# Kernel optimization log

Measured on AMD Instinct MI355X. Metric: run time of the kernel, lower is better.

Reference implementation:

```python
import jax, jax.numpy as jnp
import numpy as np

B, CDD, HIS, S, E = 16, 5, 100, 30, 256
H, V, Qd, K = 16, 16, 200, 3
R = H * V            # repr_dim = 256
T = 2 * S + 1        # transformer_length = 61
VOCAB = 50000
TAU = 0.1


def setup_inputs() -> dict:
    key = jax.random.key(0)
    ks = jax.random.split(key, 14)
    s = lambda d: float(d) ** -0.5
    return {
        "candidate_title": jax.random.randint(ks[0], (B, CDD, S), 0, VOCAB, dtype=jnp.int32),
        "clicked_title": jax.random.randint(ks[1], (B, HIS, S), 0, VOCAB, dtype=jnp.int32),
        "his_mask": jnp.zeros((B, HIS, 1), dtype=bool),
        "candidate_title_pad": jnp.ones((B, CDD, S), jnp.float32),
        "clicked_title_pad": jnp.ones((B, HIS, S), jnp.float32),
        "embedding": jax.random.normal(ks[2], (VOCAB, E), jnp.float32) * 0.1,
        "Wq_words": jax.random.normal(ks[3], (H, E, E), jnp.float32) * s(E),
        "Wv_words": jax.random.normal(ks[4], (H, E, V), jnp.float32) * s(E),
        "Wk_words": jax.random.normal(ks[5], (R, Qd), jnp.float32) * s(R),
        "bk_words": jnp.zeros((Qd,), jnp.float32),
        "query_words": jax.random.normal(ks[6], (1, Qd), jnp.float32),
        "Wq_itrs": jax.random.normal(ks[7], (H, R, R), jnp.float32) * s(R),
        "Wv_itrs": jax.random.normal(ks[8], (H, R, V), jnp.float32) * s(R),
        "Wk_itrs": jax.random.normal(ks[9], (R, Qd), jnp.float32) * s(R),
        "bk_itrs": jnp.zeros((Qd,), jnp.float32),
        "query_itrs": jax.random.normal(ks[10], (1, Qd), jnp.float32),
        "W_ltr": jax.random.normal(ks[11], (R, 1), jnp.float32) * s(R),
        "b_ltr": jnp.zeros((1,), jnp.float32),
    }


def _mhsa(x, Wq, Wv, Wk, bk, qvec):
    """Batched multi-head self-attention + additive pooling.
    x: [..., L, D]; Wq: [H, D, D]; Wv: [H, D, V]; Wk: [H*V, Qd]; qvec: [1, Qd].
    NOTE: original always scales by 1/sqrt(embedding_dim), even in mode 2.
    """
    scale = 1.0 / jnp.sqrt(jnp.asarray(E, x.dtype))
    q = jnp.einsum('...ld,hde->h...le', x, Wq)                     # per-head query
    attn = jax.nn.softmax(jnp.einsum('h...le,...me->h...lm', q, x) * scale, axis=-1)
    ctx = jnp.einsum('h...lm,...md->h...ld', attn, x)
    val = jnp.einsum('h...ld,hdv->...lhv', ctx, Wv)                # head-major concat
    mv = val.reshape(val.shape[:-2] + (H * V,))                    # [..., L, R]
    keyp = jnp.tanh(mv @ Wk + bk)                                  # [..., L, Qd]
    w = jax.nn.softmax((keyp @ qvec[0]) * scale, axis=-1)          # additive attn [..., L]
    return jnp.einsum('...l,...lr->...r', w, mv), mv


def reference(candidate_title, clicked_title, his_mask, candidate_title_pad,
              clicked_title_pad, embedding, Wq_words, Wv_words, Wk_words,
              bk_words, query_words, Wq_itrs, Wv_itrs, Wk_itrs, bk_itrs,
              query_itrs, W_ltr, b_ltr):
    # news encoding (dropout_p = 0 -> identity)
    cdd_repr, cdd_emb = _mhsa(embedding[candidate_title], Wq_words, Wv_words,
                              Wk_words, bk_words, query_words)     # [B,CDD,R], [B,CDD,S,R]
    his_repr, his_emb = _mhsa(embedding[clicked_title], Wq_words, Wv_words,
                              Wk_words, bk_words, query_words)     # [B,HIS,R], [B,HIS,S,R]

    # news-level attention with greedy gumbel top-k selection
    logits = jnp.einsum('bcr,bhr->bch', cdd_repr, his_repr)        # [B,CDD,HIS]
    logits = jnp.where(jnp.swapaxes(his_mask, -1, -2), -jnp.inf, logits)
    gkey = jax.random.key(42)
    his_flat = his_emb.reshape(B, HIS, S * R)
    acts = []
    for i in range(K):
        g = jax.random.gumbel(jax.random.fold_in(gkey, i), logits.shape, logits.dtype)
        y = jax.nn.softmax((logits + g) / TAU, axis=-1)
        hard = jax.nn.one_hot(jnp.argmax(y, -1), HIS, dtype=y.dtype)
        focus = hard - jax.lax.stop_gradient(y) + y                # straight-through
        acts.append(jnp.einsum('bch,bhx->bcx', focus, his_flat).reshape(B, CDD, S, R))
        logits = jnp.where(hard > 0, -jnp.inf, logits)
    his_act = jnp.stack(acts, axis=2)                              # [B,CDD,K,S,R]

    # fusion: candidate words | zero separator | activated history words
    fusion = jnp.zeros((B, CDD, K, T, R), his_act.dtype)
    fusion = fusion.at[..., :S, :].set(jnp.broadcast_to(cdd_emb[:, :, None], (B, CDD, K, S, R)))
    fusion = fusion.at[..., S + 1:, :].set(his_act)
    fvec, _ = _mhsa(fusion, Wq_itrs, Wv_itrs, Wk_itrs, bk_itrs, query_itrs)  # [B,CDD,K,R]
    fvec = fvec.mean(axis=2)                                       # [B,CDD,R]

    score = (fvec @ W_ltr + b_ltr)[..., 0]                         # [B,CDD]
    return jax.nn.log_softmax(score, axis=1)
```

## Files before the change

### kernel.cpp

```cpp
#include <hip/hip_runtime.h>
#include <hip/hip_bf16.h>
#include <stdint.h>

#define BB    16
#define CDD   5
#define HIS   100
#define SS    30
#define EE    256
#define HH    16
#define VV    16
#define QD    200
#define KK    3
#define TT    61
#define NCAND 80
#define NITEM 1680
#define NFUS  240

typedef __attribute__((ext_vector_type(8))) short bf16x8;
typedef __attribute__((ext_vector_type(4))) float f32x4;
#define MFMA16(a, b, c) __builtin_amdgcn_mfma_f32_16x16x32_bf16(a, b, c, 0, 0, 0)

__device__ __forceinline__ int SWZ(int l, int c) { return l * 256 + (((c) ^ (l & 7)) << 2); }
__device__ __forceinline__ int SWZW(int l, int c) {
    return l * 256 + (((c ^ (l & 7) ^ ((l & 24) >> 1))) << 2);
}

__device__ __forceinline__ float dot4(float4 a, float4 b) {
    return a.x * b.x + a.y * b.y + a.z * b.z + a.w * b.w;
}
__device__ __forceinline__ uint32_t f2bf(float x) {
    uint32_t u = __float_as_uint(x);
    return (u + 0x7fffu + ((u >> 16) & 1u)) >> 16;
}
__device__ __forceinline__ uint32_t splitpack(float x) {
    uint32_t hb = f2bf(x);
    float hf = __uint_as_float(hb << 16);
    uint32_t lb = f2bf(x - hf);
    return (hb << 16) | lb;
}
union b8u4 { uint4 u; bf16x8 b; };
__device__ __forceinline__ bf16x8 hi8(uint4 a, uint4 b) {
    b8u4 cv;
    cv.u.x = (a.x >> 16) | (a.y & 0xffff0000u);
    cv.u.y = (a.z >> 16) | (a.w & 0xffff0000u);
    cv.u.z = (b.x >> 16) | (b.y & 0xffff0000u);
    cv.u.w = (b.z >> 16) | (b.w & 0xffff0000u);
    return cv.b;
}
__device__ __forceinline__ bf16x8 lo8(uint4 a, uint4 b) {
    b8u4 cv;
    cv.u.x = (a.x & 0xffffu) | (a.y << 16);
    cv.u.y = (a.z & 0xffffu) | (a.w << 16);
    cv.u.z = (b.x & 0xffffu) | (b.y << 16);
    cv.u.w = (b.z & 0xffffu) | (b.w << 16);
    return cv.b;
}

__device__ __forceinline__ uint32_t rotl32(uint32_t v, int r) {
    return (v << r) | (v >> (32 - r));
}
__device__ __forceinline__ void tf2x32(uint32_t k0, uint32_t k1, uint32_t& x0, uint32_t& x1) {
    uint32_t k2 = k0 ^ k1 ^ 0x1BD11BDAu;
    x0 += k0; x1 += k1;
    const int r0[4] = {13, 15, 26, 6}, r1[4] = {17, 29, 16, 24};
    #pragma unroll
    for (int i = 0; i < 4; ++i) { x0 += x1; x1 = rotl32(x1, r0[i]); x1 ^= x0; }
    x0 += k1; x1 += k2 + 1u;
    #pragma unroll
    for (int i = 0; i < 4; ++i) { x0 += x1; x1 = rotl32(x1, r1[i]); x1 ^= x0; }
    x0 += k2; x1 += k0 + 2u;
    #pragma unroll
    for (int i = 0; i < 4; ++i) { x0 += x1; x1 = rotl32(x1, r0[i]); x1 ^= x0; }
    x0 += k0; x1 += k1 + 3u;
    #pragma unroll
    for (int i = 0; i < 4; ++i) { x0 += x1; x1 = rotl32(x1, r1[i]); x1 ^= x0; }
    x0 += k1; x1 += k2 + 4u;
    #pragma unroll
    for (int i = 0; i < 4; ++i) { x0 += x1; x1 = rotl32(x1, r0[i]); x1 ^= x0; }
    x0 += k2; x1 += k0 + 5u;
}

__global__ __launch_bounds__(256) void ktrans(const float* __restrict__ Wk,
                                              float* __restrict__ WkT) {
    int j = blockIdx.x;
    int r = threadIdx.x;
    WkT[j * 256 + r] = Wk[r * QD + j];
}

__global__ __launch_bounds__(256) void kprep(const float* __restrict__ W,
                                             uint16_t* __restrict__ WF) {
    const int hkt = blockIdx.x;
    const int h = hkt >> 3, kt = hkt & 7;
    const int tid = threadIdx.x;
    const int l = tid & 63, nq = tid >> 6;
    const int g = l >> 4, ml = l & 15;
    for (int t = 0; t < 4; ++t) {
        int nt = nq * 4 + t;
        uint16_t* dst = WF + (((size_t)(h * 8 + kt) * 16 + nt) * 64 + l) * 16;
        #pragma unroll
        for (int i = 0; i < 8; ++i) {
            float x = W[(size_t)h * 65536 + (size_t)(kt * 32 + g * 8 + i) * 256 + nt * 16 + ml];
            uint32_t hb = f2bf(x);
            float hf = __uint_as_float(hb << 16);
            uint32_t lb = f2bf(x - hf);
            dst[i] = (uint16_t)hb;
            dst[8 + i] = (uint16_t)lb;
        }
    }
}

__global__ __launch_bounds__(64) void kprepv(const float* __restrict__ Wv,
                                             uint16_t* __restrict__ WF) {
    const int hkt = blockIdx.x;
    const int h = hkt >> 3, kt = hkt & 7;
    const int l = threadIdx.x;
    const int g = l >> 4, ml = l & 15;
    uint16_t* dst = WF + ((size_t)hkt * 64 + l) * 16;
    #pragma unroll
    for (int i = 0; i < 8; ++i) {
        float x = Wv[((size_t)h * 256 + kt * 32 + g * 8 + i) * 16 + ml];
        uint32_t hb = f2bf(x);
        float hf = __uint_as_float(hb << 16);
        uint32_t lb = f2bf(x - hf);
        dst[i] = (uint16_t)hb;
        dst[8 + i] = (uint16_t)lb;
    }
}

__global__ __launch_bounds__(256) void kword(
    const int* __restrict__ cand, const int* __restrict__ clk,
    const float* __restrict__ emb, const uint16_t* __restrict__ Wfrag,
    const uint16_t* __restrict__ WvF, const float* __restrict__ WkT,
    const float* __restrict__ bk, const float* __restrict__ qv,
    float* __restrict__ mv_out, float* __restrict__ repr_out)
{
    __shared__ __align__(16) uint32_t xsb[32 * 256];
    __shared__ __align__(16) uint32_t qs[32 * 256];
    __shared__ __align__(16) float ps[SS * 33];
    __shared__ __align__(16) float xv[32 * VV];
    __shared__ float scr[32];
    __shared__ float wts[32];

    const int item = blockIdx.x;
    const int tid  = threadIdx.x;
    const int w    = tid >> 6, lane = tid & 63;
    const int g    = lane >> 4, ml = lane & 15;
    const int* tok = (item < NCAND) ? cand + item * SS : clk + (item - NCAND) * SS;

    for (int p = tid; p < 32 * 64; p += 256) {
        int l = p >> 6, c = p & 63;
        float4 v = make_float4(0.f, 0.f, 0.f, 0.f);
        if (l < SS) v = *(const float4*)&emb[(size_t)tok[l] * EE + 4 * c];
        uint4 s;
        s.x = splitpack(v.x); s.y = splitpack(v.y);
        s.z = splitpack(v.z); s.w = splitpack(v.w);
        *(uint4*)&xsb[SWZW(l, c)] = s;
    }
    __syncthreads();

    float* mvg = mv_out + (size_t)item * SS * EE;

    for (int h = 0; h < HH; ++h) {
        {
            f32x4 acc[2][4];
            #pragma unroll
            for (int a = 0; a < 2; ++a)
                #pragma unroll
                for (int b = 0; b < 4; ++b) acc[a][b] = (f32x4){0.f, 0.f, 0.f, 0.f};
            const uint16_t* WH = Wfrag + (size_t)h * (8 * 16 * 64 * 16);
            for (int kt = 0; kt < 8; ++kt) {
                bf16x8 ah[2], al[2];
                #pragma unroll
                for (int mt = 0; mt < 2; ++mt) {
                    int row = mt * 16 + ml;
                    int c0 = kt * 8 + 2 * g;
                    uint4 A0 = *(const uint4*)&xsb[SWZW(row, c0)];
                    uint4 A1 = *(const uint4*)&xsb[SWZW(row, c0 + 1)];
                    ah[mt] = hi8(A0, A1);
                    al[mt] = lo8(A0, A1);
                }
                #pragma unroll
                for (int n2 = 0; n2 < 4; ++n2) {
                    const uint16_t* bp = WH + (((size_t)kt * 16 + (w * 4 + n2)) * 64 + lane) * 16;
                    bf16x8 bh = *(const bf16x8*)bp;
                    bf16x8 bl = *(const bf16x8*)(bp + 8);
                    #pragma unroll
                    for (int mt = 0; mt < 2; ++mt) {
                        acc[mt][n2] = MFMA16(ah[mt], bh, acc[mt][n2]);
                        acc[mt][n2] = MFMA16(al[mt], bh, acc[mt][n2]);
                        acc[mt][n2] = MFMA16(ah[mt], bl, acc[mt][n2]);
                        acc[mt][n2] = MFMA16(al[mt], bl, acc[mt][n2]);
                    }
                }
            }
            #pragma unroll
            for (int mt = 0; mt < 2; ++mt)
                #pragma unroll
                for (int n2 = 0; n2 < 4; ++n2) {
                    int col = (w * 4 + n2) * 16 + ml;
                    int chunk = col >> 2, sub = col & 3;
                    #pragma unroll
                    for (int r = 0; r < 4; ++r) {
                        int row = mt * 16 + g * 4 + r;
                        qs[row * 256 + (((chunk ^ (row & 7) ^ ((row & 24) >> 1)) << 2) | sub)] =
                            splitpack(acc[mt][n2][r]);
                    }
                }
        }
        __syncthreads();

        if (w < 2) {
            f32x4 accs[2];
            accs[0] = (f32x4){0.f, 0.f, 0.f, 0.f};
            accs[1] = (f32x4){0.f, 0.f, 0.f, 0.f};
            const int arow = 16 * w + ml;
            for (int kt = 0; kt < 8; ++kt) {
                int c0 = kt * 8 + 2 * g;
                uint4 Q0 = *(const uint4*)&qs[SWZW(arow, c0)];
                uint4 Q1 = *(const uint4*)&qs[SWZW(arow, c0 + 1)];
                bf16x8 qh = hi8(Q0, Q1), ql = lo8(Q0, Q1);
                #pragma unroll
                for (int nt = 0; nt < 2; ++nt) {
                    int brow = nt * 16 + ml;
                    uint4 X0 = *(const uint4*)&xsb[SWZW(brow, c0)];
                    uint4 X1 = *(const uint4*)&xsb[SWZW(brow, c0 + 1)];
                    bf16x8 xh = hi8(X0, X1), xl = lo8(X0, X1);
                    accs[nt] = MFMA16(qh, xh, accs[nt]);
                    accs[nt] = MFMA16(ql, xh, accs[nt]);
                    accs[nt] = MFMA16(qh, xl, accs[nt]);
                }
            }
            #pragma unroll
            for (int r = 0; r < 4; ++r) {
                float v0 = accs[0][r] * 0.0625f;
                float v1 = (ml < 14) ? accs[1][r] * 0.0625f : -INFINITY;
                float mx = fmaxf(v0, v1);
                mx = fmaxf(mx, __shfl_xor(mx, 1));
                mx = fmaxf(mx, __shfl_xor(mx, 2));
                mx = fmaxf(mx, __shfl_xor(mx, 4));
                mx = fmaxf(mx, __shfl_xor(mx, 8));
                float e0 = expf(v0 - mx);
                float e1 = (ml < 14) ? expf(v1 - mx) : 0.f;
                float s = e0 + e1;
                s += __shfl_xor(s, 1); s += __shfl_xor(s, 2);
                s += __shfl_xor(s, 4); s += __shfl_xor(s, 8);
                float inv = 1.f / s;
                int lrow = 16 * w + 4 * g + r;
                if (lrow < SS) {
                    ps[lrow * 33 + ml] = e0 * inv;
                    if (ml < 14) ps[lrow * 33 + 16 + ml] = e1 * inv;
                }
            }
        } else {
            f32x4 accv = (f32x4){0.f, 0.f, 0.f, 0.f};
            const int mt = w - 2;
            const int arow = 16 * mt + ml;
            for (int kt = 0; kt < 8; ++kt) {
                int c0 = kt * 8 + 2 * g;
                uint4 A0 = *(const uint4*)&xsb[SWZW(arow, c0)];
                uint4 A1 = *(const uint4*)&xsb[SWZW(arow, c0 + 1)];
                bf16x8 ah = hi8(A0, A1), al = lo8(A0, A1);
                const uint16_t* bp = WvF + (((size_t)h * 8 + kt) * 64 + lane) * 16;
                bf16x8 bh = *(const bf16x8*)bp;
                bf16x8 bl = *(const bf16x8*)(bp + 8);
                accv = MFMA16(ah, bh, accv);
                accv = MFMA16(al, bh, accv);
                accv = MFMA16(ah, bl, accv);
            }
            #pragma unroll
            for (int r = 0; r < 4; ++r) {
                int m = 16 * mt + 4 * g + r;
                if (m < SS) xv[m * 16 + ml] = accv[r];
            }
        }
        __syncthreads();

        if (tid < SS * 4) {
            const int l = tid >> 2, vq = tid & 3;
            float4 a = make_float4(0.f, 0.f, 0.f, 0.f);
            for (int m = 0; m < SS; ++m) {
                float pw = ps[l * 33 + m];
                float4 v4 = *(const float4*)&xv[m * 16 + vq * 4];
                a.x += pw * v4.x; a.y += pw * v4.y; a.z += pw * v4.z; a.w += pw * v4.w;
            }
            *(float4*)&mvg[l * 256 + h * 16 + vq * 4] = a;
        }
    }

    __threadfence();
    __syncthreads();
    float* kq = (float*)qs;
    if (tid < 200) {
        const int jq = tid % 50, lg = tid / 50;
        const int j0 = jq * 4;
        const int r0 = lg * 8;
        const int nr = (lg == 3) ? 6 : 8;
        float4 a[8];
        #pragma unroll
        for (int r = 0; r < 8; ++r) a[r] = make_float4(bk[j0], bk[j0+1], bk[j0+2], bk[j0+3]);
        for (int c = 0; c < 64; ++c) {
            float4 w0 = *(const float4*)&WkT[(j0 + 0) * 256 + 4 * c];
            float4 w1 = *(const float4*)&WkT[(j0 + 1) * 256 + 4 * c];
            float4 w2 = *(const float4*)&WkT[(j0 + 2) * 256 + 4 * c];
            float4 w3 = *(const float4*)&WkT[(j0 + 3) * 256 + 4 * c];
            #pragma unroll
            for (int r = 0; r < 8; ++r) {
                if (r < nr) {
                    float4 m4 = *(const float4*)&mvg[(r0 + r) * 256 + 4 * c];
                    a[r].x += dot4(m4, w0);
                    a[r].y += dot4(m4, w1);
                    a[r].z += dot4(m4, w2);
                    a[r].w += dot4(m4, w3);
                }
            }
        }
        #pragma unroll
        for (int r = 0; r < 8; ++r) {
            if (r < nr) {
                int row = r0 + r;
                kq[row * 204 + j0 + 0] = tanhf(a[r].x) * qv[j0 + 0];
                kq[row * 204 + j0 + 1] = tanhf(a[r].y) * qv[j0 + 1];
                kq[row * 204 + j0 + 2] = tanhf(a[r].z) * qv[j0 + 2];
                kq[row * 204 + j0 + 3] = tanhf(a[r].w) * qv[j0 + 3];
            }
        }
    }
    __syncthreads();
    if (tid < SS) {
        float a = 0.f;
        for (int j = 0; j < QD; ++j) a += kq[tid * 204 + j];
        scr[tid] = a * 0.0625f;
    }
    __syncthreads();
    if (tid == 0) {
        float mx = -INFINITY;
        for (int l = 0; l < SS; ++l) mx = fmaxf(mx, scr[l]);
        float sum = 0.f;
        for (int l = 0; l < SS; ++l) { float ev = expf(scr[l] - mx); wts[l] = ev; sum += ev; }
        float inv = 1.f / sum;
        for (int l = 0; l < SS; ++l) wts[l] *= inv;
    }
    __syncthreads();
    {
        float a = 0.f;
        for (int l = 0; l < SS; ++l) a += wts[l] * mvg[l * 256 + tid];
        repr_out[(size_t)item * EE + tid] = a;
    }
}

__global__ __launch_bounds__(128) void klogit(
    const float* __restrict__ repr, float* __restrict__ logits)
{
    const int bc = blockIdx.x;
    const int b  = bc / CDD;
    const int tid = threadIdx.x;
    __shared__ float cr[EE];
    for (int e = tid; e < EE; e += 128) cr[e] = repr[(size_t)bc * EE + e];
    __syncthreads();
    for (int h = tid; h < HIS; h += 128) {
        const float* hr = repr + (size_t)(NCAND + b * HIS + h) * EE;
        float a = 0.f;
        for (int e = 0; e < EE; ++e) a += cr[e] * hr[e];
        logits[bc * HIS + h] = a;
    }
}

__global__ __launch_bounds__(128) void ksel(
    const float* __restrict__ logits, int* __restrict__ sel)
{
    const int bc = blockIdx.x, tid = threadIdx.x;
    __shared__ float lg[HIS];
    __shared__ float pert[HIS];
    for (int h = tid; h < HIS; h += 128) lg[h] = logits[bc * HIS + h];
    __syncthreads();
    for (int i = 0; i < KK; ++i) {
        uint32_t c0 = 0u, c1 = (uint32_t)i;
        tf2x32(0u, 42u, c0, c1);
        for (int h = tid; h < HIS; h += 128) {
            int n = bc * HIS + h;
            uint32_t x0, x1; int lane;
            if (n < 4000) { x0 = (uint32_t)n;          x1 = (uint32_t)(n + 4000); lane = 0; }
            else          { x0 = (uint32_t)(n - 4000); x1 = (uint32_t)n;          lane = 1; }
            tf2x32(c0, c1, x0, x1);
            uint32_t bits = lane ? x1 : x0;
            float f = __uint_as_float((bits >> 9) | 0x3F800000u) - 1.0f;
            const float TINY = 1.17549435e-38f;
            float u = fmaxf(f + TINY, TINY);
            float g = -logf(-logf(u));
            pert[h] = lg[h] + g;
        }
        __syncthreads();
        if (tid == 0) {
            float best = -INFINITY; int bi = 0;
            for (int h = 0; h < HIS; ++h)
                if (pert[h] > best) { best = pert[h]; bi = h; }
            sel[bc * KK + i] = bi;
            lg[bi] = -INFINITY;
        }
        __syncthreads();
    }
}

__global__ __launch_bounds__(256) void kfus(
    const float* __restrict__ mv, const int* __restrict__ sel,
    const uint16_t* __restrict__ Wfrag, const uint16_t* __restrict__ WvF,
    float* __restrict__ mvf)
{
    __shared__ __align__(16) uint32_t xsb[64 * 256];
    __shared__ __align__(16) uint16_t qsb[64 * 256];
    __shared__ __align__(16) float ps[64 * 65];
    __shared__ __align__(16) float xv[64 * 16];

    const int item = blockIdx.x;
    const int tid  = threadIdx.x;
    const int w    = tid >> 6, lane = tid & 63;
    const int g    = lane >> 4, ml = lane & 15;
    const int bc = item / KK, k = item - bc * KK;
    const int b  = bc / CDD;
    const int sh = sel[bc * KK + k];
    const float* cmv = mv + (size_t)bc * SS * EE;
    const float* hmv = mv + (size_t)(NCAND + b * HIS + sh) * SS * EE;
    float* out = mvf + (size_t)item * TT * EE;

    for (int p = tid; p < 64 * 64; p += 256) {
        int l = p >> 6, c = p & 63;
        float4 v = make_float4(0.f, 0.f, 0.f, 0.f);
        if (l < SS)                v = *(const float4*)&cmv[l * 256 + 4 * c];
        else if (l > SS && l < TT) v = *(const float4*)&hmv[(l - SS - 1) * 256 + 4 * c];
        uint4 s;
        s.x = splitpack(v.x); s.y = splitpack(v.y);
        s.z = splitpack(v.z); s.w = splitpack(v.w);
        *(uint4*)&xsb[SWZ(l, c)] = s;
    }
    __syncthreads();

    for (int h = 0; h < HH; ++h) {
        {
            f32x4 acc[4][4];
            #pragma unroll
            for (int a = 0; a < 4; ++a)
                #pragma unroll
                for (int b2 = 0; b2 < 4; ++b2) acc[a][b2] = (f32x4){0.f, 0.f, 0.f, 0.f};
            const uint16_t* WH = Wfrag + (size_t)h * (8 * 16 * 64 * 16);
            for (int kt = 0; kt < 8; ++kt) {
                bf16x8 ah[4], al[4];
                #pragma unroll
                for (int mt = 0; mt < 4; ++mt) {
                    int row = mt * 16 + ml;
                    int c0 = kt * 8 + 2 * g;
                    uint4 A0 = *(const uint4*)&xsb[SWZ(row, c0)];
                    uint4 A1 = *(const uint4*)&xsb[SWZ(row, c0 + 1)];
                    ah[mt] = hi8(A0, A1);
                    al[mt] = lo8(A0, A1);
                }
                #pragma unroll
                for (int n2 = 0; n2 < 4; ++n2) {
                    const uint16_t* bp = WH + (((size_t)kt * 16 + (w * 4 + n2)) * 64 + lane) * 16;
                    bf16x8 bh = *(const bf16x8*)bp;
                    bf16x8 bl = *(const bf16x8*)(bp + 8);
                    #pragma unroll
                    for (int mt = 0; mt < 4; ++mt) {
                        acc[mt][n2] = MFMA16(ah[mt], bh, acc[mt][n2]);
                        acc[mt][n2] = MFMA16(al[mt], bh, acc[mt][n2]);
                        acc[mt][n2] = MFMA16(ah[mt], bl, acc[mt][n2]);
                    }
                }
            }
            #pragma unroll
            for (int mt = 0; mt < 4; ++mt)
                #pragma unroll
                for (int n2 = 0; n2 < 4; ++n2) {
                    #pragma unroll
                    for (int r = 0; r < 4; ++r) {
                        uint32_t mb = f2bf(acc[mt][n2][r]);
                        uint32_t ob = (uint32_t)__shfl_xor((int)mb, 1);
                        if ((ml & 1) == 0) {
                            int col0 = (w * 4 + n2) * 16 + ml;
                            int row = mt * 16 + g * 4 + r;
                            int idx = row * 256 + ((((col0 >> 3) ^ (row & 7)) << 3) | (col0 & 7));
                            *(uint32_t*)&qsb[idx] = mb | (ob << 16);
                        }
                    }
                }
        }
        __syncthreads();

        {
            f32x4 accs[4];
            #pragma unroll
            for (int nt = 0; nt < 4; ++nt) accs[nt] = (f32x4){0.f, 0.f, 0.f, 0.f};
            f32x4 accv = (f32x4){0.f, 0.f, 0.f, 0.f};
            const int arow = 16 * w + ml;
            for (int kt = 0; kt < 8; ++kt) {
                int cq = 4 * kt + g;
                bf16x8 qh = *(const bf16x8*)&qsb[arow * 256 + ((cq ^ (arow & 7)) << 3)];
                int c0 = kt * 8 + 2 * g;
                #pragma unroll
                for (int nt = 0; nt < 4; ++nt) {
                    int brow = 16 * nt + ml;
                    uint4 X0 = *(const uint4*)&xsb[SWZ(brow, c0)];
                    uint4 X1 = *(const uint4*)&xsb[SWZ(brow, c0 + 1)];
                    accs[nt] = MFMA16(qh, hi8(X0, X1), accs[nt]);
                }
                uint4 A0 = *(const uint4*)&xsb[SWZ(arow, c0)];
                uint4 A1 = *(const uint4*)&xsb[SWZ(arow, c0 + 1)];
                bf16x8 bh = *(const bf16x8*)&WvF[(((size_t)h * 8 + kt) * 64 + lane) * 16];
                accv = MFMA16(hi8(A0, A1), bh, accv);
            }
            #pragma unroll
            for (int r = 0; r < 4; ++r) {
                float v0 = accs[0][r] * 0.0625f;
                float v1 = accs[1][r] * 0.0625f;
                float v2 = accs[2][r] * 0.0625f;
                float v3 = (ml < 13) ? accs[3][r] * 0.0625f : -INFINITY;
                float mx = fmaxf(fmaxf(v0, v1), fmaxf(v2, v3));
                mx = fmaxf(mx, __shfl_xor(mx, 1));
                mx = fmaxf(mx, __shfl_xor(mx, 2));
                mx = fmaxf(mx, __shfl_xor(mx, 4));
                mx = fmaxf(mx, __shfl_xor(mx, 8));
                float e0 = expf(v0 - mx);
                float e1 = expf(v1 - mx);
                float e2 = expf(v2 - mx);
                float e3 = (ml < 13) ? expf(v3 - mx) : 0.f;
                float s = e0 + e1 + e2 + e3;
                s += __shfl_xor(s, 1); s += __shfl_xor(s, 2);
                s += __shfl_xor(s, 4); s += __shfl_xor(s, 8);
                float inv = 1.f / s;
                int lrow = 16 * w + 4 * g + r;
                if (lrow < TT) {
                    ps[lrow * 65 + ml]      = e0 * inv;
                    ps[lrow * 65 + 16 + ml] = e1 * inv;
                    ps[lrow * 65 + 32 + ml] = e2 * inv;
                    if (ml < 13) ps[lrow * 65 + 48 + ml] = e3 * inv;
                }
                int m = 16 * w + 4 * g + r;
                if (m < TT) xv[m * 16 + ml] = accv[r];
            }
        }
        __syncthreads();

        if (lane < TT) {
            const int l = lane, vq = w;
            float4 a = make_float4(0.f, 0.f, 0.f, 0.f);
            for (int m = 0; m < TT; ++m) {
                float pw = ps[l * 65 + m];
                float4 x4 = *(const float4*)&xv[m * 16 + vq * 4];
                a.x += pw * x4.x; a.y += pw * x4.y; a.z += pw * x4.z; a.w += pw * x4.w;
            }
            *(float4*)&out[l * 256 + h * 16 + vq * 4] = a;
        }
    }
}

__global__ __launch_bounds__(256) void kpoolf(
    const float* __restrict__ mvf, const float* __restrict__ WkT,
    const float* __restrict__ bk, const float* __restrict__ qv,
    float* __restrict__ fvec)
{
    __shared__ float kq[TT * 201];
    __shared__ float scr[TT];
    __shared__ float wts[TT];
    const int item = blockIdx.x, tid = threadIdx.x;
    const float* src = mvf + (size_t)item * TT * EE;
    for (int p = tid; p < TT * 50; p += 256) {
        int l = p / 50, jq = p - l * 50;
        int j0 = jq * 4;
        float4 a = make_float4(bk[j0], bk[j0+1], bk[j0+2], bk[j0+3]);
        const float* mr = src + l * 256;
        for (int c = 0; c < 64; ++c) {
            float4 m4 = *(const float4*)&mr[4 * c];
            a.x += dot4(m4, *(const float4*)&WkT[(j0+0) * 256 + 4*c]);
            a.y += dot4(m4, *(const float4*)&WkT[(j0+1) * 256 + 4*c]);
            a.z += dot4(m4, *(const float4*)&WkT[(j0+2) * 256 + 4*c]);
            a.w += dot4(m4, *(const float4*)&WkT[(j0+3) * 256 + 4*c]);
        }
        kq[l*201 + j0 + 0] = tanhf(a.x) * qv[j0+0];
        kq[l*201 + j0 + 1] = tanhf(a.y) * qv[j0+1];
        kq[l*201 + j0 + 2] = tanhf(a.z) * qv[j0+2];
        kq[l*201 + j0 + 3] = tanhf(a.w) * qv[j0+3];
    }
    __syncthreads();
    if (tid < TT) {
        float a = 0.f;
        for (int j = 0; j < QD; ++j) a += kq[tid * 201 + j];
        scr[tid] = a * 0.0625f;
    }
    __syncthreads();
    if (tid == 0) {
        float mx = -INFINITY;
        for (int l = 0; l < TT; ++l) mx = fmaxf(mx, scr[l]);
        float sum = 0.f;
        for (int l = 0; l < TT; ++l) { float ev = expf(scr[l] - mx); wts[l] = ev; sum += ev; }
        float inv = 1.f / sum;
        for (int l = 0; l < TT; ++l) wts[l] *= inv;
    }
    __syncthreads();
    float a = 0.f;
    for (int l = 0; l < TT; ++l) a += wts[l] * src[l * 256 + tid];
    fvec[(size_t)item * EE + tid] = a;
}

__global__ __launch_bounds__(256) void kfinal(
    const float* __restrict__ fvec, const float* __restrict__ Wl,
    const float* __restrict__ bl, float* __restrict__ out)
{
    const int b = blockIdx.x, tid = threadIdx.x;
    __shared__ float red[256];
    __shared__ float sc5[CDD];
    for (int c = 0; c < CDD; ++c) {
        size_t base = ((size_t)(b * CDD + c) * KK) * EE + tid;
        float f = (fvec[base] + fvec[base + EE] + fvec[base + 2 * EE]) * (1.f / 3.f);
        red[tid] = f * Wl[tid];
        __syncthreads();
        for (int s = 128; s > 0; s >>= 1) {
            if (tid < s) red[tid] += red[tid + s];
            __syncthreads();
        }
        if (tid == 0) sc5[c] = red[0] + bl[0];
        __syncthreads();
    }
    if (tid == 0) {
        float mx = -INFINITY;
        for (int c = 0; c < CDD; ++c) mx = fmaxf(mx, sc5[c]);
        float sum = 0.f;
        for (int c = 0; c < CDD; ++c) sum += expf(sc5[c] - mx);
        float lse = mx + logf(sum);
        for (int c = 0; c < CDD; ++c) out[b * CDD + c] = sc5[c] - lse;
    }
}

extern "C" void kernel_launch(void* const* d_in, const int* in_sizes, int n_in,
                              void* d_out, int out_size, void* d_ws, size_t ws_size,
                              hipStream_t stream) {
    const int*   cand = (const int*)d_in[0];
    const int*   clk  = (const int*)d_in[1];
    const float* emb  = (const float*)d_in[5];
    const float* Wq_w = (const float*)d_in[6];
    const float* Wv_w = (const float*)d_in[7];
    const float* Wk_w = (const float*)d_in[8];
    const float* bk_w = (const float*)d_in[9];
    const float* q_w  = (const float*)d_in[10];
    const float* Wq_i = (const float*)d_in[11];
    const float* Wv_i = (const float*)d_in[12];
    const float* Wk_i = (const float*)d_in[13];
    const float* bk_i = (const float*)d_in[14];
    const float* q_i  = (const float*)d_in[15];
    const float* Wl   = (const float*)d_in[16];
    const float* bl   = (const float*)d_in[17];

    float* ws     = (float*)d_ws;
    float* mv     = ws;
    float* repr   = mv   + (size_t)NITEM * SS * EE;
    float* mvf    = repr + (size_t)NITEM * EE;
    float* fvec   = mvf  + (size_t)NFUS * TT * EE;
    float* logits = fvec + (size_t)NFUS * EE;
    float* WkTw   = logits + NCAND * HIS;
    float* WkTi   = WkTw + QD * EE;
    int*   sel    = (int*)(WkTi + QD * EE);
    uint16_t* WfW = (uint16_t*)((float*)sel + 256);
    uint16_t* WfI = WfW + (size_t)16 * 8 * 16 * 64 * 16;
    uint16_t* WvFw = WfI + (size_t)16 * 8 * 16 * 64 * 16;
    uint16_t* WvFi = WvFw + (size_t)16 * 8 * 64 * 16;

    ktrans<<<dim3(QD),    dim3(256), 0, stream>>>(Wk_w, WkTw);
    ktrans<<<dim3(QD),    dim3(256), 0, stream>>>(Wk_i, WkTi);
    kprep <<<dim3(128),   dim3(256), 0, stream>>>(Wq_w, WfW);
    kprep <<<dim3(128),   dim3(256), 0, stream>>>(Wq_i, WfI);
    kprepv<<<dim3(128),   dim3(64),  0, stream>>>(Wv_w, WvFw);
    kprepv<<<dim3(128),   dim3(64),  0, stream>>>(Wv_i, WvFi);
    kword <<<dim3(NITEM), dim3(256), 0, stream>>>(cand, clk, emb, WfW, WvFw, WkTw, bk_w, q_w, mv, repr);
    klogit<<<dim3(NCAND), dim3(128), 0, stream>>>(repr, logits);
    ksel  <<<dim3(NCAND), dim3(128), 0, stream>>>(logits, sel);
    kfus  <<<dim3(NFUS),  dim3(256), 0, stream>>>(mv, sel, WfI, WvFi, mvf);
    kpoolf<<<dim3(NFUS),  dim3(256), 0, stream>>>(mvf, WkTi, bk_i, q_i, fvec);
    kfinal<<<dim3(BB),    dim3(256), 0, stream>>>(fvec, Wl, bl, (float*)d_out);
}
```

Before: 2.151 ms.

## Pipeline per-head projection with attention and cache word fragments in registers

In the word-level attention kernel, the embedding A-fragments are loaded once into registers instead of being reloaded from shared memory for every head and every matmul. The query, score and value buffers are double-buffered so the projection for head h+1 runs in the same phase as head h's scores and values. Head h-1's probability-times-value product is deferred into that phase as well, removing one barrier per head. The x staging buffer is aliased onto the second query buffer, and the kernel now asks for 2 blocks per CU; the register-resident fragments raise VGPR pressure and risk spills or lower occupancy. A barrier is also added at the end of the per-head loop in the fusion kernel.

```diff
diff --git a/kernel.cpp b/kernel.cpp
--- a/kernel.cpp
+++ b/kernel.cpp
@@ -127,17 +127,58 @@
     }
 }
 
-__global__ __launch_bounds__(256) void kword(
+__device__ __forceinline__ void kword_A(
+    int h, uint32_t* __restrict__ qdst, const uint16_t* __restrict__ Wfrag,
+    const bf16x8 (&xah)[2][8], const bf16x8 (&xal)[2][8],
+    int w, int lane, int g, int ml)
+{
+    f32x4 acc[2][4];
+    #pragma unroll
+    for (int a = 0; a < 2; ++a)
+        #pragma unroll
+        for (int b = 0; b < 4; ++b) acc[a][b] = (f32x4){0.f, 0.f, 0.f, 0.f};
+    const uint16_t* WH = Wfrag + (size_t)h * (8 * 16 * 64 * 16);
+    #pragma unroll
+    for (int kt = 0; kt < 8; ++kt) {
+        #pragma unroll
+        for (int n2 = 0; n2 < 4; ++n2) {
+            const uint16_t* bp = WH + (((size_t)kt * 16 + (w * 4 + n2)) * 64 + lane) * 16;
+            bf16x8 bh = *(const bf16x8*)bp;
+            bf16x8 bl = *(const bf16x8*)(bp + 8);
+            #pragma unroll
+            for (int mt = 0; mt < 2; ++mt) {
+                acc[mt][n2] = MFMA16(xah[mt][kt], bh, acc[mt][n2]);
+                acc[mt][n2] = MFMA16(xal[mt][kt], bh, acc[mt][n2]);
+                acc[mt][n2] = MFMA16(xah[mt][kt], bl, acc[mt][n2]);
+                acc[mt][n2] = MFMA16(xal[mt][kt], bl, acc[mt][n2]);
+            }
+        }
+    }
+    #pragma unroll
+    for (int mt = 0; mt < 2; ++mt)
+        #pragma unroll
+        for (int n2 = 0; n2 < 4; ++n2) {
+            int col = (w * 4 + n2) * 16 + ml;
+            int chunk = col >> 2, sub = col & 3;
+            #pragma unroll
+            for (int r = 0; r < 4; ++r) {
+                int row = mt * 16 + g * 4 + r;
+                qdst[row * 256 + (((chunk ^ (row & 7) ^ ((row & 24) >> 1)) << 2) | sub)] =
+                    splitpack(acc[mt][n2][r]);
+            }
+        }
+}
+
+__global__ __launch_bounds__(256, 2) void kword(
     const int* __restrict__ cand, const int* __restrict__ clk,
     const float* __restrict__ emb, const uint16_t* __restrict__ Wfrag,
     const uint16_t* __restrict__ WvF, const float* __restrict__ WkT,
     const float* __restrict__ bk, const float* __restrict__ qv,
     float* __restrict__ mv_out, float* __restrict__ repr_out)
 {
-    __shared__ __align__(16) uint32_t xsb[32 * 256];
-    __shared__ __align__(16) uint32_t qs[32 * 256];
-    __shared__ __align__(16) float ps[SS * 33];
-    __shared__ __align__(16) float xv[32 * VV];
+    __shared__ __align__(16) uint32_t qsd[2][32 * 256];
+    __shared__ __align__(16) float ps[2][SS * 33];
+    __shared__ __align__(16) float xv[2][32 * VV];
     __shared__ float scr[32];
     __shared__ float wts[32];
 
@@ -147,6 +188,7 @@
     const int g    = lane >> 4, ml = lane & 15;
     const int* tok = (item < NCAND) ? cand + item * SS : clk + (item - NCAND) * SS;
 
+    uint32_t* xsb = qsd[1];
     for (int p = tid; p < 32 * 64; p += 256) {
         int l = p >> 6, c = p & 63;
         float4 v = make_float4(0.f, 0.f, 0.f, 0.f);
@@ -158,76 +200,42 @@
     }
     __syncthreads();
 
+    bf16x8 xah[2][8], xal[2][8];
+    #pragma unroll
+    for (int mt = 0; mt < 2; ++mt)
+        #pragma unroll
+        for (int kt = 0; kt < 8; ++kt) {
+            int row = mt * 16 + ml;
+            int c0 = kt * 8 + 2 * g;
+            uint4 A0 = *(const uint4*)&xsb[SWZW(row, c0)];
+            uint4 A1 = *(const uint4*)&xsb[SWZW(row, c0 + 1)];
+            xah[mt][kt] = hi8(A0, A1);
+            xal[mt][kt] = lo8(A0, A1);
+        }
+
     float* mvg = mv_out + (size_t)item * SS * EE;
 
+    kword_A(0, qsd[0], Wfrag, xah, xal, w, lane, g, ml);
+    __syncthreads();
+
     for (int h = 0; h < HH; ++h) {
-        {
-            f32x4 acc[2][4];
-            #pragma unroll
-            for (int a = 0; a < 2; ++a)
-                #pragma unroll
-                for (int b = 0; b < 4; ++b) acc[a][b] = (f32x4){0.f, 0.f, 0.f, 0.f};
-            const uint16_t* WH = Wfrag + (size_t)h * (8 * 16 * 64 * 16);
-            for (int kt = 0; kt < 8; ++kt) {
-                bf16x8 ah[2], al[2];
-                #pragma unroll
-                for (int mt = 0; mt < 2; ++mt) {
-                    int row = mt * 16 + ml;
-                    int c0 = kt * 8 + 2 * g;
-                    uint4 A0 = *(const uint4*)&xsb[SWZW(row, c0)];
-                    uint4 A1 = *(const uint4*)&xsb[SWZW(row, c0 + 1)];
-                    ah[mt] = hi8(A0, A1);
-                    al[mt] = lo8(A0, A1);
-                }
-                #pragma unroll
-                for (int n2 = 0; n2 < 4; ++n2) {
-                    const uint16_t* bp = WH + (((size_t)kt * 16 + (w * 4 + n2)) * 64 + lane) * 16;
-                    bf16x8 bh = *(const bf16x8*)bp;
-                    bf16x8 bl = *(const bf16x8*)(bp + 8);
-                    #pragma unroll
-                    for (int mt = 0; mt < 2; ++mt) {
-                        acc[mt][n2] = MFMA16(ah[mt], bh, acc[mt][n2]);
-                        acc[mt][n2] = MFMA16(al[mt], bh, acc[mt][n2]);
-                        acc[mt][n2] = MFMA16(ah[mt], bl, acc[mt][n2]);
-                        acc[mt][n2] = MFMA16(al[mt], bl, acc[mt][n2]);
-                    }
-                }
-            }
-            #pragma unroll
-            for (int mt = 0; mt < 2; ++mt)
-                #pragma unroll
-                for (int n2 = 0; n2 < 4; ++n2) {
-                    int col = (w * 4 + n2) * 16 + ml;
-                    int chunk = col >> 2, sub = col & 3;
-                    #pragma unroll
-                    for (int r = 0; r < 4; ++r) {
-                        int row = mt * 16 + g * 4 + r;
-                        qs[row * 256 + (((chunk ^ (row & 7) ^ ((row & 24) >> 1)) << 2) | sub)] =
-                            splitpack(acc[mt][n2][r]);
-                    }
-                }
-        }
-        __syncthreads();
-
+        const int cur = h & 1, oth = cur ^ 1;
         if (w < 2) {
             f32x4 accs[2];
             accs[0] = (f32x4){0.f, 0.f, 0.f, 0.f};
             accs[1] = (f32x4){0.f, 0.f, 0.f, 0.f};
             const int arow = 16 * w + ml;
+            #pragma unroll
             for (int kt = 0; kt < 8; ++kt) {
                 int c0 = kt * 8 + 2 * g;
-                uint4 Q0 = *(const uint4*)&qs[SWZW(arow, c0)];
-                uint4 Q1 = *(const uint4*)&qs[SWZW(arow, c0 + 1)];
+                uint4 Q0 = *(const uint4*)&qsd[cur][SWZW(arow, c0)];
+                uint4 Q1 = *(const uint4*)&qsd[cur][SWZW(arow, c0 + 1)];
                 bf16x8 qh = hi8(Q0, Q1), ql = lo8(Q0, Q1);
                 #pragma unroll
                 for (int nt = 0; nt < 2; ++nt) {
-                    int brow = nt * 16 + ml;
-                    uint4 X0 = *(const uint4*)&xsb[SWZW(brow, c0)];
-                    uint4 X1 = *(const uint4*)&xsb[SWZW(brow, c0 + 1)];
-                    bf16x8 xh = hi8(X0, X1), xl = lo8(X0, X1);
-                    accs[nt] = MFMA16(qh, xh, accs[nt]);
-                    accs[nt] = MFMA16(ql, xh, accs[nt]);
-                    accs[nt] = MFMA16(qh, xl, accs[nt]);
+                    accs[nt] = MFMA16(qh, xah[nt][kt], accs[nt]);
+                    accs[nt] = MFMA16(ql, xah[nt][kt], accs[nt]);
+                    accs[nt] = MFMA16(qh, xal[nt][kt], accs[nt]);
                 }
             }
             #pragma unroll
@@ -247,49 +255,65 @@
                 float inv = 1.f / s;
                 int lrow = 16 * w + 4 * g + r;
                 if (lrow < SS) {
-                    ps[lrow * 33 + ml] = e0 * inv;
-                    if (ml < 14) ps[lrow * 33 + 16 + ml] = e1 * inv;
+                    ps[cur][lrow * 33 + ml] = e0 * inv;
+                    if (ml < 14) ps[cur][lrow * 33 + 16 + ml] = e1 * inv;
                 }
             }
         } else {
             f32x4 accv = (f32x4){0.f, 0.f, 0.f, 0.f};
             const int mt = w - 2;
-            const int arow = 16 * mt + ml;
+            #pragma unroll
             for (int kt = 0; kt < 8; ++kt) {
-                int c0 = kt * 8 + 2 * g;
-                uint4 A0 = *(const uint4*)&xsb[SWZW(arow, c0)];
-                uint4 A1 = *(const uint4*)&xsb[SWZW(arow, c0 + 1)];
-                bf16x8 ah = hi8(A0, A1), al = lo8(A0, A1);
                 const uint16_t* bp = WvF + (((size_t)h * 8 + kt) * 64 + lane) * 16;
                 bf16x8 bh = *(const bf16x8*)bp;
                 bf16x8 bl = *(const bf16x8*)(bp + 8);
-                accv = MFMA16(ah, bh, accv);
-                accv = MFMA16(al, bh, accv);
-                accv = MFMA16(ah, bl, accv);
+                accv = MFMA16(xah[mt][kt], bh, accv);
+                accv = MFMA16(xal[mt][kt], bh, accv);
+                accv = MFMA16(xah[mt][kt], bl, accv);
             }
             #pragma unroll
             for (int r = 0; r < 4; ++r) {
                 int m = 16 * mt + 4 * g + r;
-                if (m < SS) xv[m * 16 + ml] = accv[r];
-            }
-        }
+                if (m < SS) xv[cur][m * 16 + ml] = accv[r];
+            }
+            if (h > 0) {
+                const int id = tid - 128;
+                if (id < SS * 4) {
+                    const int l = id >> 2, vq = id & 3;
+                    float4 a = make_float4(0.f, 0.f, 0.f, 0.f);
+                    for (int m = 0; m < SS; ++m) {
+                        float pw = ps[oth][l * 33 + m];
+                        float4 v4 = *(const float4*)&xv[oth][m * 16 + vq * 4];
+                        a.x += pw * v4.x; a.y += pw * v4.y;
+                        a.z += pw * v4.z; a.w += pw * v4.w;
+                    }
+                    *(float4*)&mvg[l * 256 + (h - 1) * 16 + vq * 4] = a;
+                }
+            }
+        }
+        if (h < HH - 1)
+            kword_A(h + 1, qsd[oth], Wfrag, xah, xal, w, lane, g, ml);
         __syncthreads();
-
-        if (tid < SS * 4) {
-            const int l = tid >> 2, vq = tid & 3;
+    }
+
+    if (w >= 2) {
+        const int id = tid - 128;
+        if (id < SS * 4) {
+            const int l = id >> 2, vq = id & 3;
             float4 a = make_float4(0.f, 0.f, 0.f, 0.f);
             for (int m = 0; m < SS; ++m) {
-                float pw = ps[l * 33 + m];
-                float4 v4 = *(const float4*)&xv[m * 16 + vq * 4];
-                a.x += pw * v4.x; a.y += pw * v4.y; a.z += pw * v4.z; a.w += pw * v4.w;
-            }
-            *(float4*)&mvg[l * 256 + h * 16 + vq * 4] = a;
+                float pw = ps[1][l * 33 + m];
+                float4 v4 = *(const float4*)&xv[1][m * 16 + vq * 4];
+                a.x += pw * v4.x; a.y += pw * v4.y;
+                a.z += pw * v4.z; a.w += pw * v4.w;
+            }
+            *(float4*)&mvg[l * 256 + 15 * 16 + vq * 4] = a;
         }
     }
 
     __threadfence();
     __syncthreads();
-    float* kq = (float*)qs;
+    float* kq = (float*)qsd[0];
     if (tid < 200) {
         const int jq = tid % 50, lg = tid / 50;
         const int j0 = jq * 4;
@@ -549,6 +573,7 @@
             }
             *(float4*)&out[l * 256 + h * 16 + vq * 4] = a;
         }
+        __syncthreads();
     }
 }
 
```

New measurement: 2.614 ms. +21.5%, slower.
